# Kernel tuning notes

Hardware: AMD Instinct MI355X
Metric: run time of the kernel (lower is better)

The kernel has to match this reference:

```python
import jax, jax.numpy as jnp
import numpy as np

B, T, ENC_DIM, QUERY_DIM = 64, 2000, 512, 1024
UNITS, FILTERS, KERNEL = 128, 32, 31


def setup_inputs() -> dict:
    key = jax.random.key(0)
    ks = jax.random.split(key, 12)
    prev = jax.random.uniform(ks[1], (B, T), dtype=jnp.float32)
    prev = prev / jnp.sum(prev, axis=-1, keepdims=True)  # alignment-like
    return {
        "query": jax.random.normal(ks[0], (B, QUERY_DIM), dtype=jnp.float32),
        "previous_alignments": prev,
        "memory": jax.random.normal(ks[2], (B, T, ENC_DIM), dtype=jnp.float32),
        "memory_sequence_length": jax.random.randint(ks[3], (B,), T // 2, T + 1, dtype=jnp.int32),
        "W_query": jax.random.normal(ks[4], (QUERY_DIM, UNITS), dtype=jnp.float32) * 0.02,
        "W_keys": jax.random.normal(ks[5], (ENC_DIM, UNITS), dtype=jnp.float32) * 0.02,
        "conv_w": jax.random.normal(ks[6], (KERNEL, 1, FILTERS), dtype=jnp.float32) * 0.02,
        "conv_b": jnp.zeros((FILTERS,), dtype=jnp.float32),
        "W_loc": jax.random.normal(ks[7], (FILTERS, UNITS), dtype=jnp.float32) * 0.02,
        "v_a": jax.random.normal(ks[8], (UNITS,), dtype=jnp.float32) * 0.1,
        "b_a": jnp.zeros((UNITS,), dtype=jnp.float32),
    }


def reference(query, previous_alignments, memory, memory_sequence_length,
              W_query, W_keys, conv_w, conv_b, W_loc, v_a, b_a):
    # keys: precomputed projection of memory  [B, T, units]
    keys = jnp.einsum('bte,eu->btu', memory, W_keys)
    # processed query  [B, 1, units]
    pq = (query @ W_query)[:, None, :]
    # location features: conv1d 'same' over previous alignments  [B, T, filters]
    loc = jax.lax.conv_general_dilated(
        previous_alignments[:, :, None], conv_w,
        window_strides=(1,), padding='SAME',
        dimension_numbers=('NWC', 'WIO', 'NWC')) + conv_b
    pl = jnp.einsum('btf,fu->btu', loc, W_loc)
    # additive energy  [B, T]
    energy = jnp.einsum('u,btu->bt', v_a, jnp.tanh(keys + pq + pl + b_a))
    # mask positions beyond sequence length
    mask = jnp.arange(T)[None, :] < memory_sequence_length[:, None]
    energy = jnp.where(mask, energy, -1e9)
    alignments = jax.nn.softmax(energy, axis=-1)
    next_state = alignments + previous_alignments  # cumulative_weights=True
    return alignments, next_state
```

## Files before the change

### kernel.cpp

```cpp
#include <hip/hip_runtime.h>
#include <math.h>

#define B_   64
#define T_   2000
#define ENC_ 512
#define QD_  1024
#define U_   128
#define F_   32
#define KW_  31

typedef __bf16 bf16x8 __attribute__((ext_vector_type(8)));
typedef float  f32x4  __attribute__((ext_vector_type(4)));

__device__ __forceinline__ __bf16 f2bf(float f) { return (__bf16)f; }

__global__ __launch_bounds__(1024)
void prep_bias(const float* __restrict__ query, const float* __restrict__ Wq,
               const float* __restrict__ conv_b, const float* __restrict__ Wloc,
               const float* __restrict__ b_a, float* __restrict__ bias)
{
    int b = blockIdx.x;
    int u = threadIdx.x & 127;
    int q = threadIdx.x >> 7;
    const float* qr = query + b * QD_;
    float acc = 0.f;
    for (int e = q * 128; e < q * 128 + 128; ++e)
        acc = fmaf(qr[e], Wq[e * U_ + u], acc);
    __shared__ float red[1024];
    red[threadIdx.x] = acc;
    __syncthreads();
    if (q == 0) {
        float s = 0.f;
        #pragma unroll
        for (int i = 0; i < 8; ++i) s += red[i * 128 + u];
        float cb = 0.f;
        for (int f = 0; f < F_; ++f)
            cb = fmaf(conv_b[f], Wloc[f * U_ + u], cb);
        bias[b * U_ + u] = s + cb + b_a[u];
    }
}

__global__ __launch_bounds__(256)
void prep_wb(const float* __restrict__ Wk, const float* __restrict__ conv_w,
             const float* __restrict__ Wloc, __bf16* __restrict__ wsB)
{
    int idx = blockIdx.x * 256 + threadIdx.x;
    if (idx >= 17 * 8 * 64) return;
    int lane = idx & 63;
    int nt   = (idx >> 6) & 7;
    int kk   = idx >> 9;
    int n = nt * 16 + (lane & 15);
    int kbase = (lane >> 4) * 8;
    float vals[8];
    if (kk < 16) {
        #pragma unroll
        for (int j = 0; j < 8; ++j)
            vals[j] = Wk[(kk * 32 + kbase + j) * U_ + n];
    } else {
        #pragma unroll
        for (int j = 0; j < 8; ++j) {
            int k = kbase + j;
            float s = 0.f;
            if (k < KW_)
                for (int f = 0; f < F_; ++f)
                    s = fmaf(conv_w[k * F_ + f], Wloc[f * U_ + n], s);
            vals[j] = s;
        }
    }
    __bf16* dst = wsB + (size_t)idx * 8;
    #pragma unroll
    for (int j = 0; j < 8; ++j) dst[j] = f2bf(vals[j]);
}

__global__ __launch_bounds__(256)
void lsa_energy(const float* __restrict__ mem, const float* __restrict__ prev,
                const float* __restrict__ bias, const bf16x8* __restrict__ wsB,
                const float* __restrict__ v_a, float* __restrict__ energy)
{
    const int tile = blockIdx.x & 15;
    const int b    = blockIdx.x >> 4;
    const int t0   = tile * 128;
    const int tid  = threadIdx.x;
    const int wave = tid >> 6;
    const int lane = tid & 63;
    const int l15  = lane & 15;
    const int quad = lane >> 4;

    __shared__ float lds_prev[160];
    __shared__ float lds_bias[U_];
    __shared__ float lds_v[U_];

    if (tid < 160) {
        int t = t0 - 15 + tid;
        float v = 0.f;
        if (tid < 158 && t >= 0 && t < T_) v = prev[b * T_ + t];
        lds_prev[tid] = v;
    }
    if (tid < U_)                 lds_bias[tid] = bias[b * U_ + tid];
    if (tid >= U_ && tid < 2*U_)  lds_v[tid - U_] = v_a[tid - U_];
    __syncthreads();

    f32x4 acc[2][8];
    #pragma unroll
    for (int s = 0; s < 2; ++s)
        #pragma unroll
        for (int n = 0; n < 8; ++n) acc[s][n] = (f32x4){0.f, 0.f, 0.f, 0.f};

    const int rl0 = wave * 32 + l15;
    int r0 = t0 + rl0;      if (r0 > T_ - 1) r0 = T_ - 1;
    int r1 = t0 + rl0 + 16; if (r1 > T_ - 1) r1 = T_ - 1;
    const float* A0 = mem + ((size_t)b * T_ + r0) * ENC_ + quad * 8;
    const float* A1 = mem + ((size_t)b * T_ + r1) * ENC_ + quad * 8;

    for (int kk = 0; kk < 16; ++kk) {
        bf16x8 bfr[8];
        const bf16x8* bp = wsB + (size_t)(kk * 8) * 64 + lane;
        #pragma unroll
        for (int n = 0; n < 8; ++n) bfr[n] = bp[n * 64];

        const float* p0 = A0 + kk * 32;
        const float* p1 = A1 + kk * 32;
        float4 x0 = *(const float4*)p0, y0 = *(const float4*)(p0 + 4);
        float4 x1 = *(const float4*)p1, y1 = *(const float4*)(p1 + 4);
        bf16x8 a0, a1;
        a0[0]=f2bf(x0.x); a0[1]=f2bf(x0.y); a0[2]=f2bf(x0.z); a0[3]=f2bf(x0.w);
        a0[4]=f2bf(y0.x); a0[5]=f2bf(y0.y); a0[6]=f2bf(y0.z); a0[7]=f2bf(y0.w);
        a1[0]=f2bf(x1.x); a1[1]=f2bf(x1.y); a1[2]=f2bf(x1.z); a1[3]=f2bf(x1.w);
        a1[4]=f2bf(y1.x); a1[5]=f2bf(y1.y); a1[6]=f2bf(y1.z); a1[7]=f2bf(y1.w);

        #pragma unroll
        for (int n = 0; n < 8; ++n) {
            acc[0][n] = __builtin_amdgcn_mfma_f32_16x16x32_bf16(a0, bfr[n], acc[0][n], 0, 0, 0);
            acc[1][n] = __builtin_amdgcn_mfma_f32_16x16x32_bf16(a1, bfr[n], acc[1][n], 0, 0, 0);
        }
    }

    {
        bf16x8 bfr[8];
        const bf16x8* bp = wsB + (size_t)(16 * 8) * 64 + lane;
        #pragma unroll
        for (int n = 0; n < 8; ++n) bfr[n] = bp[n * 64];
        bf16x8 a0, a1;
        int base = rl0 + quad * 8;
        #pragma unroll
        for (int j = 0; j < 8; ++j) a0[j] = f2bf(lds_prev[base + j]);
        #pragma unroll
        for (int j = 0; j < 8; ++j) a1[j] = f2bf(lds_prev[base + 16 + j]);
        #pragma unroll
        for (int n = 0; n < 8; ++n) {
            acc[0][n] = __builtin_amdgcn_mfma_f32_16x16x32_bf16(a0, bfr[n], acc[0][n], 0, 0, 0);
            acc[1][n] = __builtin_amdgcn_mfma_f32_16x16x32_bf16(a1, bfr[n], acc[1][n], 0, 0, 0);
        }
    }

    float part[2][4] = {{0.f,0.f,0.f,0.f},{0.f,0.f,0.f,0.f}};
    #pragma unroll
    for (int n = 0; n < 8; ++n) {
        float bb = lds_bias[n * 16 + l15];
        float vv = lds_v[n * 16 + l15];
        #pragma unroll
        for (int s = 0; s < 2; ++s)
            #pragma unroll
            for (int i = 0; i < 4; ++i) {
                float x  = acc[s][n][i] + bb;
                float ax = __builtin_fabsf(x);
                float e  = __expf(-2.f * ax);
                float th = (1.f - e) / (1.f + e);
                part[s][i] += (x < 0.f ? -th : th) * vv;
            }
    }
    #pragma unroll
    for (int s = 0; s < 2; ++s)
        #pragma unroll
        for (int i = 0; i < 4; ++i) {
            float p = part[s][i];
            p += __shfl_xor(p, 1);
            p += __shfl_xor(p, 2);
            p += __shfl_xor(p, 4);
            p += __shfl_xor(p, 8);
            part[s][i] = p;
        }
    if (l15 == 0) {
        #pragma unroll
        for (int s = 0; s < 2; ++s)
            #pragma unroll
            for (int i = 0; i < 4; ++i) {
                int t = t0 + wave * 32 + s * 16 + quad * 4 + i;
                if (t < T_) energy[b * T_ + t] = part[s][i];
            }
    }
}

__global__ __launch_bounds__(256)
void lsa_softmax(const float* __restrict__ prev, const int* __restrict__ seqlen,
                 float* __restrict__ out)
{
    int b = blockIdx.x;
    int tid = threadIdx.x;
    int len = seqlen[b];
    float e[8];
    float m = -1e30f;
    #pragma unroll
    for (int i = 0; i < 8; ++i) {
        int t = tid + i * 256;
        float x = -1e30f;
        if (t < T_) {
            x = out[b * T_ + t];
            if (t >= len) x = -1e9f;
        }
        e[i] = x;
        m = fmaxf(m, x);
    }
    #pragma unroll
    for (int off = 32; off >= 1; off >>= 1) m = fmaxf(m, __shfl_xor(m, off));
    __shared__ float wmax[4], wsum[4];
    if ((tid & 63) == 0) wmax[tid >> 6] = m;
    __syncthreads();
    m = fmaxf(fmaxf(wmax[0], wmax[1]), fmaxf(wmax[2], wmax[3]));
    float s = 0.f;
    #pragma unroll
    for (int i = 0; i < 8; ++i) {
        float p = __expf(e[i] - m);
        if (tid + i * 256 >= T_) p = 0.f;
        e[i] = p;
        s += p;
    }
    #pragma unroll
    for (int off = 32; off >= 1; off >>= 1) s += __shfl_xor(s, off);
    if ((tid & 63) == 0) wsum[tid >> 6] = s;
    __syncthreads();
    s = wsum[0] + wsum[1] + wsum[2] + wsum[3];
    float inv = 1.f / s;
    #pragma unroll
    for (int i = 0; i < 8; ++i) {
        int t = tid + i * 256;
        if (t < T_) {
            float a = e[i] * inv;
            out[b * T_ + t] = a;
            out[(size_t)B_ * T_ + b * T_ + t] = a + prev[b * T_ + t];
        }
    }
}

extern "C" void kernel_launch(void* const* d_in, const int* in_sizes, int n_in,
                              void* d_out, int out_size, void* d_ws, size_t ws_size,
                              hipStream_t stream)
{
    const float* query  = (const float*)d_in[0];
    const float* prev   = (const float*)d_in[1];
    const float* memory = (const float*)d_in[2];
    const int*   mlen   = (const int*)d_in[3];
    const float* Wq     = (const float*)d_in[4];
    const float* Wk     = (const float*)d_in[5];
    const float* conv_w = (const float*)d_in[6];
    const float* conv_b = (const float*)d_in[7];
    const float* Wloc   = (const float*)d_in[8];
    const float* v_a    = (const float*)d_in[9];
    const float* b_a    = (const float*)d_in[10];
    float* out = (float*)d_out;

    __bf16* wsB  = (__bf16*)d_ws;
    float*  bias = (float*)((char*)d_ws + (size_t)17 * 8 * 64 * 8 * 2);

    prep_bias<<<dim3(64), dim3(1024), 0, stream>>>(query, Wq, conv_b, Wloc, b_a, bias);
    prep_wb<<<dim3(34), dim3(256), 0, stream>>>(Wk, conv_w, Wloc, wsB);
    lsa_energy<<<dim3(64 * 16), dim3(256), 0, stream>>>(memory, prev, bias,
                                                        (const bf16x8*)wsB, v_a, out);
    lsa_softmax<<<dim3(64), dim3(256), 0, stream>>>(prev, mlen, out);
}
```

Baseline: 447.9 us.

## Skip masked time tiles, merge prep kernels, split weight-fragment loads

The energy kernel now reads memory_sequence_length and returns early for 128-step tiles that start past the sequence length, since softmax masks those positions anyway. This avoids reading memory and running MFMA work for padded regions. The two prep kernels are merged into one launch with a reworked query-projection reduction. The energy kernel also loads the B-weight fragments in two halves of four and gains a launch_bounds occupancy hint, aimed at lowering register pressure. The change depends on the softmax kernel ignoring the stale energy values left in skipped tiles.

Measured after the change: 401.5 us. -10.4%, faster.

```diff
diff --git a/kernel.cpp b/kernel.cpp
--- a/kernel.cpp
+++ b/kernel.cpp
@@ -14,72 +14,78 @@
 
 __device__ __forceinline__ __bf16 f2bf(float f) { return (__bf16)f; }
 
-__global__ __launch_bounds__(1024)
-void prep_bias(const float* __restrict__ query, const float* __restrict__ Wq,
-               const float* __restrict__ conv_b, const float* __restrict__ Wloc,
-               const float* __restrict__ b_a, float* __restrict__ bias)
-{
-    int b = blockIdx.x;
-    int u = threadIdx.x & 127;
-    int q = threadIdx.x >> 7;
-    const float* qr = query + b * QD_;
-    float acc = 0.f;
-    for (int e = q * 128; e < q * 128 + 128; ++e)
-        acc = fmaf(qr[e], Wq[e * U_ + u], acc);
-    __shared__ float red[1024];
-    red[threadIdx.x] = acc;
-    __syncthreads();
-    if (q == 0) {
-        float s = 0.f;
-        #pragma unroll
-        for (int i = 0; i < 8; ++i) s += red[i * 128 + u];
-        float cb = 0.f;
-        for (int f = 0; f < F_; ++f)
-            cb = fmaf(conv_b[f], Wloc[f * U_ + u], cb);
-        bias[b * U_ + u] = s + cb + b_a[u];
-    }
-}
-
 __global__ __launch_bounds__(256)
-void prep_wb(const float* __restrict__ Wk, const float* __restrict__ conv_w,
-             const float* __restrict__ Wloc, __bf16* __restrict__ wsB)
-{
-    int idx = blockIdx.x * 256 + threadIdx.x;
-    if (idx >= 17 * 8 * 64) return;
-    int lane = idx & 63;
-    int nt   = (idx >> 6) & 7;
-    int kk   = idx >> 9;
-    int n = nt * 16 + (lane & 15);
-    int kbase = (lane >> 4) * 8;
-    float vals[8];
-    if (kk < 16) {
-        #pragma unroll
-        for (int j = 0; j < 8; ++j)
-            vals[j] = Wk[(kk * 32 + kbase + j) * U_ + n];
+void prep(const float* __restrict__ query, const float* __restrict__ Wq,
+          const float* __restrict__ conv_b, const float* __restrict__ Wloc,
+          const float* __restrict__ b_a, const float* __restrict__ Wk,
+          const float* __restrict__ conv_w,
+          float* __restrict__ bias, __bf16* __restrict__ wsB)
+{
+    const int tid = threadIdx.x;
+    if (blockIdx.x < 64) {
+        int b = blockIdx.x;
+        int u = tid & 127;
+        int h = tid >> 7;
+        const float* qr = query + b * QD_ + h * 512;
+        const float* wq = Wq + (size_t)(h * 512) * U_ + u;
+        float a0 = 0.f, a1 = 0.f, a2 = 0.f, a3 = 0.f;
+        for (int e = 0; e < 512; e += 4) {
+            a0 = fmaf(qr[e + 0], wq[(size_t)(e + 0) * U_], a0);
+            a1 = fmaf(qr[e + 1], wq[(size_t)(e + 1) * U_], a1);
+            a2 = fmaf(qr[e + 2], wq[(size_t)(e + 2) * U_], a2);
+            a3 = fmaf(qr[e + 3], wq[(size_t)(e + 3) * U_], a3);
+        }
+        __shared__ float red[256];
+        red[tid] = (a0 + a1) + (a2 + a3);
+        __syncthreads();
+        if (h == 0) {
+            float s = red[u] + red[128 + u];
+            float cb = 0.f;
+            for (int f = 0; f < F_; ++f)
+                cb = fmaf(conv_b[f], Wloc[f * U_ + u], cb);
+            bias[b * U_ + u] = s + cb + b_a[u];
+        }
     } else {
-        #pragma unroll
-        for (int j = 0; j < 8; ++j) {
-            int k = kbase + j;
-            float s = 0.f;
-            if (k < KW_)
-                for (int f = 0; f < F_; ++f)
-                    s = fmaf(conv_w[k * F_ + f], Wloc[f * U_ + n], s);
-            vals[j] = s;
-        }
-    }
-    __bf16* dst = wsB + (size_t)idx * 8;
-    #pragma unroll
-    for (int j = 0; j < 8; ++j) dst[j] = f2bf(vals[j]);
-}
-
-__global__ __launch_bounds__(256)
+        int idx = (blockIdx.x - 64) * 256 + tid;
+        if (idx >= 17 * 8 * 64) return;
+        int lane = idx & 63;
+        int nt   = (idx >> 6) & 7;
+        int kk   = idx >> 9;
+        int n = nt * 16 + (lane & 15);
+        int kbase = (lane >> 4) * 8;
+        float vals[8];
+        if (kk < 16) {
+            #pragma unroll
+            for (int j = 0; j < 8; ++j)
+                vals[j] = Wk[(size_t)(kk * 32 + kbase + j) * U_ + n];
+        } else {
+            #pragma unroll
+            for (int j = 0; j < 8; ++j) {
+                int k = kbase + j;
+                float s = 0.f;
+                if (k < KW_)
+                    for (int f = 0; f < F_; ++f)
+                        s = fmaf(conv_w[k * F_ + f], Wloc[f * U_ + n], s);
+                vals[j] = s;
+            }
+        }
+        __bf16* dst = wsB + (size_t)idx * 8;
+        #pragma unroll
+        for (int j = 0; j < 8; ++j) dst[j] = f2bf(vals[j]);
+    }
+}
+
+__global__ __launch_bounds__(256, 4)
 void lsa_energy(const float* __restrict__ mem, const float* __restrict__ prev,
                 const float* __restrict__ bias, const bf16x8* __restrict__ wsB,
-                const float* __restrict__ v_a, float* __restrict__ energy)
+                const float* __restrict__ v_a, const int* __restrict__ seqlen,
+                float* __restrict__ energy)
 {
     const int tile = blockIdx.x & 15;
     const int b    = blockIdx.x >> 4;
     const int t0   = tile * 128;
+    if (t0 >= seqlen[b]) return;
+
     const int tid  = threadIdx.x;
     const int wave = tid >> 6;
     const int lane = tid & 63;
@@ -109,47 +115,59 @@
     const int rl0 = wave * 32 + l15;
     int r0 = t0 + rl0;      if (r0 > T_ - 1) r0 = T_ - 1;
     int r1 = t0 + rl0 + 16; if (r1 > T_ - 1) r1 = T_ - 1;
-    const float* A0 = mem + ((size_t)b * T_ + r0) * ENC_ + quad * 8;
-    const float* A1 = mem + ((size_t)b * T_ + r1) * ENC_ + quad * 8;
+    const float* pA0 = mem + ((size_t)b * T_ + r0) * ENC_ + quad * 8;
+    const float* pA1 = mem + ((size_t)b * T_ + r1) * ENC_ + quad * 8;
+    const bf16x8* bp = wsB + lane;
 
     for (int kk = 0; kk < 16; ++kk) {
-        bf16x8 bfr[8];
-        const bf16x8* bp = wsB + (size_t)(kk * 8) * 64 + lane;
-        #pragma unroll
-        for (int n = 0; n < 8; ++n) bfr[n] = bp[n * 64];
-
-        const float* p0 = A0 + kk * 32;
-        const float* p1 = A1 + kk * 32;
-        float4 x0 = *(const float4*)p0, y0 = *(const float4*)(p0 + 4);
-        float4 x1 = *(const float4*)p1, y1 = *(const float4*)(p1 + 4);
+        float4 x0 = *(const float4*)pA0, y0 = *(const float4*)(pA0 + 4);
+        float4 x1 = *(const float4*)pA1, y1 = *(const float4*)(pA1 + 4);
+        pA0 += 32; pA1 += 32;
         bf16x8 a0, a1;
         a0[0]=f2bf(x0.x); a0[1]=f2bf(x0.y); a0[2]=f2bf(x0.z); a0[3]=f2bf(x0.w);
         a0[4]=f2bf(y0.x); a0[5]=f2bf(y0.y); a0[6]=f2bf(y0.z); a0[7]=f2bf(y0.w);
         a1[0]=f2bf(x1.x); a1[1]=f2bf(x1.y); a1[2]=f2bf(x1.z); a1[3]=f2bf(x1.w);
         a1[4]=f2bf(y1.x); a1[5]=f2bf(y1.y); a1[6]=f2bf(y1.z); a1[7]=f2bf(y1.w);
 
-        #pragma unroll
-        for (int n = 0; n < 8; ++n) {
+        bf16x8 bfr[4];
+        #pragma unroll
+        for (int n = 0; n < 4; ++n) bfr[n] = bp[n * 64];
+        #pragma unroll
+        for (int n = 0; n < 4; ++n) {
             acc[0][n] = __builtin_amdgcn_mfma_f32_16x16x32_bf16(a0, bfr[n], acc[0][n], 0, 0, 0);
             acc[1][n] = __builtin_amdgcn_mfma_f32_16x16x32_bf16(a1, bfr[n], acc[1][n], 0, 0, 0);
         }
+        #pragma unroll
+        for (int n = 0; n < 4; ++n) bfr[n] = bp[(n + 4) * 64];
+        #pragma unroll
+        for (int n = 0; n < 4; ++n) {
+            acc[0][n+4] = __builtin_amdgcn_mfma_f32_16x16x32_bf16(a0, bfr[n], acc[0][n+4], 0, 0, 0);
+            acc[1][n+4] = __builtin_amdgcn_mfma_f32_16x16x32_bf16(a1, bfr[n], acc[1][n+4], 0, 0, 0);
+        }
+        bp += 8 * 64;
     }
 
     {
-        bf16x8 bfr[8];
-        const bf16x8* bp = wsB + (size_t)(16 * 8) * 64 + lane;
-        #pragma unroll
-        for (int n = 0; n < 8; ++n) bfr[n] = bp[n * 64];
         bf16x8 a0, a1;
         int base = rl0 + quad * 8;
         #pragma unroll
         for (int j = 0; j < 8; ++j) a0[j] = f2bf(lds_prev[base + j]);
         #pragma unroll
         for (int j = 0; j < 8; ++j) a1[j] = f2bf(lds_prev[base + 16 + j]);
-        #pragma unroll
-        for (int n = 0; n < 8; ++n) {
+        bf16x8 bfr[4];
+        #pragma unroll
+        for (int n = 0; n < 4; ++n) bfr[n] = bp[n * 64];
+        #pragma unroll
+        for (int n = 0; n < 4; ++n) {
             acc[0][n] = __builtin_amdgcn_mfma_f32_16x16x32_bf16(a0, bfr[n], acc[0][n], 0, 0, 0);
             acc[1][n] = __builtin_amdgcn_mfma_f32_16x16x32_bf16(a1, bfr[n], acc[1][n], 0, 0, 0);
+        }
+        #pragma unroll
+        for (int n = 0; n < 4; ++n) bfr[n] = bp[(n + 4) * 64];
+        #pragma unroll
+        for (int n = 0; n < 4; ++n) {
+            acc[0][n+4] = __builtin_amdgcn_mfma_f32_16x16x32_bf16(a0, bfr[n], acc[0][n+4], 0, 0, 0);
+            acc[1][n+4] = __builtin_amdgcn_mfma_f32_16x16x32_bf16(a1, bfr[n], acc[1][n+4], 0, 0, 0);
         }
     }
 
@@ -262,9 +280,10 @@
     __bf16* wsB  = (__bf16*)d_ws;
     float*  bias = (float*)((char*)d_ws + (size_t)17 * 8 * 64 * 8 * 2);
 
-    prep_bias<<<dim3(64), dim3(1024), 0, stream>>>(query, Wq, conv_b, Wloc, b_a, bias);
-    prep_wb<<<dim3(34), dim3(256), 0, stream>>>(Wk, conv_w, Wloc, wsB);
+    prep<<<dim3(98), dim3(256), 0, stream>>>(query, Wq, conv_b, Wloc, b_a,
+                                             Wk, conv_w, bias, wsB);
     lsa_energy<<<dim3(64 * 16), dim3(256), 0, stream>>>(memory, prev, bias,
-                                                        (const bf16x8*)wsB, v_a, out);
+                                                        (const bf16x8*)wsB,
+                                                        v_a, mlen, out);
     lsa_softmax<<<dim3(64), dim3(256), 0, stream>>>(prev, mlen, out);
 }
```
